# Optimization experiments

Measured on AMD Instinct MI355X. Metric: run time of the kernel, lower is better.

Reference implementation:

```python
import jax, jax.numpy as jnp
import numpy as np

NUM_HEADS = 16


def setup_inputs() -> dict:
    key = jax.random.key(0)
    k1, k2, k3 = jax.random.split(key, 3)
    B, S, D = 4, 2048, 1024
    x = jax.random.normal(k1, (B, S, D), dtype=jnp.float32)
    w_qkv = jax.random.normal(k2, (D, 3 * D), dtype=jnp.float32) * 0.02
    b_qkv = jnp.zeros((3 * D,), dtype=jnp.float32)
    w_proj = jax.random.normal(k3, (D, D), dtype=jnp.float32) * 0.02
    b_proj = jnp.zeros((D,), dtype=jnp.float32)
    return {"x": x, "w_qkv": w_qkv, "b_qkv": b_qkv, "w_proj": w_proj, "b_proj": b_proj}


def reference(x, w_qkv, b_qkv, w_proj, b_proj):
    B, S, D = x.shape
    H = NUM_HEADS
    hd = D // H
    # fused qkv projection: [B,S,3D] -> [B,S,3H,hd]
    qkv = (x @ w_qkv + b_qkv).reshape(B, S, 3 * H, hd)
    q, k, v = jnp.split(qkv, 3, axis=2)  # each [B,S,H,hd]
    scale = (1.0 / jnp.sqrt(hd)).astype(x.dtype)
    scores = jnp.einsum("bqhd,bkhd->bhqk", q, k) * scale  # [B,H,S,S]
    causal = jnp.tril(jnp.ones((S, S), dtype=bool))  # [S,S]
    masked = jnp.where(causal, scores, jnp.finfo(scores.dtype).min)
    # softmax in fp32 reduce dtype, cast back (dropout_rate=0 -> identity)
    attn = jax.nn.softmax(masked.astype(jnp.float32)).astype(masked.dtype)
    out = jnp.einsum("bhqk,bkhd->bqhd", attn, v).reshape(B, S, D)
    return out @ w_proj + b_proj
```

## Files before the change

### kernel.cpp

```cpp
#include <hip/hip_runtime.h>
#include <hip/hip_bf16.h>

typedef __attribute__((ext_vector_type(8))) short short8;
typedef __attribute__((ext_vector_type(4))) float f32x4;

#define B_   4
#define S_   2048
#define D_   1024
#define H_   16
#define HD_  64
#define M_   (B_ * S_)
#define N3_  (3 * D_)

#define GLDS16(g, l)                                                        \
  __builtin_amdgcn_global_load_lds(                                         \
      (const __attribute__((address_space(1))) void*)(g),                   \
      (__attribute__((address_space(3))) void*)(l), 16, 0, 0)

__device__ __forceinline__ unsigned pack_bf2(float a, float b) {
  union { __hip_bfloat16 h; unsigned short s; } ua, ub;
  ua.h = __float2bfloat16(a);
  ub.h = __float2bfloat16(b);
  return (unsigned)ua.s | ((unsigned)ub.s << 16);
}

__global__ __launch_bounds__(256) void cast_f32_bf16(
    const float* __restrict__ in, __hip_bfloat16* __restrict__ out, int n) {
  int i = (blockIdx.x * 256 + threadIdx.x) * 4;
  if (i + 3 < n) {
    float4 v = *(const float4*)(in + i);
    union { ushort4 u4; __hip_bfloat16 h[4]; } p;
    p.h[0] = __float2bfloat16(v.x);
    p.h[1] = __float2bfloat16(v.y);
    p.h[2] = __float2bfloat16(v.z);
    p.h[3] = __float2bfloat16(v.w);
    *(ushort4*)(out + i) = p.u4;
  }
}

__global__ __launch_bounds__(256) void transpose_cast(
    const float* __restrict__ in, __hip_bfloat16* __restrict__ out,
    int rows, int cols) {
  __shared__ float tile[32][33];
  int bx = blockIdx.x * 32;
  int by = blockIdx.y * 32;
  int tx = threadIdx.x, ty = threadIdx.y;
#pragma unroll
  for (int i = 0; i < 4; ++i)
    tile[ty + i * 8][tx] = in[(size_t)(by + ty + i * 8) * cols + bx + tx];
  __syncthreads();
#pragma unroll
  for (int i = 0; i < 4; ++i)
    out[(size_t)(bx + ty + i * 8) * rows + by + tx] =
        __float2bfloat16(tile[tx][ty + i * 8]);
}

__device__ inline void store_out(float* p, float v) { *p = v; }
__device__ inline void store_out(__hip_bfloat16* p, float v) {
  *p = __float2bfloat16(v);
}

template <typename OUT_T, bool WVT>
__global__ __launch_bounds__(256) void gemm_bt_bias(
    const __hip_bfloat16* __restrict__ A, const __hip_bfloat16* __restrict__ Bt,
    const float* __restrict__ bias, OUT_T* __restrict__ C,
    __hip_bfloat16* __restrict__ vt, int M, int N, int K) {
  __shared__ __align__(16) __hip_bfloat16 Alds[128 * 64];
  __shared__ __align__(16) __hip_bfloat16 Blds[128 * 64];
  const int t = threadIdx.x;
  const int wave = t >> 6, lane = t & 63;
  const int quad = lane >> 4, l15 = lane & 15;
  const int wm = (wave >> 1) * 64, wn = (wave & 1) * 64;
  const int m0 = blockIdx.y * 128, n0 = blockIdx.x * 128;

  const int rsub = lane >> 3;
  const int gc16 = (lane & 7) ^ (rsub & 7);
  const __hip_bfloat16* gA[4];
  const __hip_bfloat16* gB[4];
  __hip_bfloat16* lA[4];
  __hip_bfloat16* lB[4];
#pragma unroll
  for (int i = 0; i < 4; ++i) {
    int c = wave * 4 + i;
    int row = c * 8 + rsub;
    gA[i] = A + (size_t)(m0 + row) * K + gc16 * 8;
    gB[i] = Bt + (size_t)(n0 + row) * K + gc16 * 8;
    lA[i] = Alds + c * 512;
    lB[i] = Blds + c * 512;
  }

  f32x4 acc[4][4] = {};

  for (int k0 = 0; k0 < K; k0 += 64) {
#pragma unroll
    for (int i = 0; i < 4; ++i) {
      GLDS16(gA[i] + k0, lA[i]);
      GLDS16(gB[i] + k0, lB[i]);
    }
    __syncthreads();
#pragma unroll
    for (int kk = 0; kk < 2; ++kk) {
      const int fo = ((kk * 4 + quad) ^ (l15 & 7)) * 8;
      short8 a[4], bfr[4];
#pragma unroll
      for (int mt = 0; mt < 4; ++mt)
        a[mt] = *(const short8*)(Alds + (wm + mt * 16 + l15) * 64 + fo);
#pragma unroll
      for (int nt = 0; nt < 4; ++nt)
        bfr[nt] = *(const short8*)(Blds + (wn + nt * 16 + l15) * 64 + fo);
#pragma unroll
      for (int mt = 0; mt < 4; ++mt)
#pragma unroll
        for (int nt = 0; nt < 4; ++nt)
          acc[mt][nt] = __builtin_amdgcn_mfma_f32_16x16x32_bf16(
              a[mt], bfr[nt], acc[mt][nt], 0, 0, 0);
    }
    __syncthreads();
  }

  if (WVT && n0 >= 2048) {
#pragma unroll
    for (int mt = 0; mt < 4; ++mt)
#pragma unroll
      for (int nt = 0; nt < 4; ++nt) {
        int col = n0 + wn + nt * 16 + l15;
        float bv = bias[col];
        int hv = (col - 2048) >> 6, d = (col - 2048) & 63;
        int row0 = m0 + wm + mt * 16 + quad * 4;
        int bidx = row0 >> 11, s = row0 & 2047;
        uint2 w;
        w.x = pack_bf2(acc[mt][nt][0] + bv, acc[mt][nt][1] + bv);
        w.y = pack_bf2(acc[mt][nt][2] + bv, acc[mt][nt][3] + bv);
        *(uint2*)(vt + ((size_t)(bidx * 16 + hv) * 64 + d) * 2048 + s) = w;
      }
  } else {
#pragma unroll
    for (int mt = 0; mt < 4; ++mt)
#pragma unroll
      for (int nt = 0; nt < 4; ++nt) {
        int col = n0 + wn + nt * 16 + l15;
        float bv = bias[col];
#pragma unroll
        for (int r = 0; r < 4; ++r) {
          int row = m0 + wm + mt * 16 + quad * 4 + r;
          store_out(C + (size_t)row * N + col, acc[mt][nt][r] + bv);
        }
      }
  }
}

__global__ __launch_bounds__(128, 3) void attn_causal(
    const __hip_bfloat16* __restrict__ qkv,
    const __hip_bfloat16* __restrict__ vt,
    __hip_bfloat16* __restrict__ ctx) {
  __shared__ __align__(16) __hip_bfloat16 Klds[64 * 64];
  __shared__ __align__(16) __hip_bfloat16 Vlds[64 * 64];
  __shared__ __align__(16) __hip_bfloat16 Plds[2][2][16][64];

  const int t = threadIdx.x;
  const int wave = t >> 6, lane = t & 63;
  const int quad = lane >> 4, l15 = lane & 15;
  const int qb = 31 - (int)blockIdx.x;
  const int h = blockIdx.y, b = blockIdx.z;

  const size_t qbase = (size_t)b * S_ * N3_ + h * HD_;
  const size_t kbase = qbase + D_;
  const size_t vtbase = (size_t)(b * H_ + h) * HD_ * S_;
  const float C2 = 0.18033688f;

  short8 ones;
#pragma unroll
  for (int j = 0; j < 8; ++j) ones[j] = (short)0x3F80;

  short8 qf[2][2];
#pragma unroll
  for (int g = 0; g < 2; ++g) {
    const int qrow = qb * 64 + wave * 32 + g * 16 + l15;
    qf[g][0] = *(const short8*)(qkv + qbase + (size_t)qrow * N3_ + quad * 8);
    qf[g][1] =
        *(const short8*)(qkv + qbase + (size_t)qrow * N3_ + 32 + quad * 8);
  }

  const int rsub = lane >> 3;
  const int swz = ((lane & 7) ^ rsub) * 8;
  const __hip_bfloat16* gK[4];
  const __hip_bfloat16* gV[4];
  __hip_bfloat16* lK[4];
  __hip_bfloat16* lV[4];
#pragma unroll
  for (int i = 0; i < 4; ++i) {
    const int c = wave * 4 + i;
    gK[i] = qkv + kbase + (size_t)(c * 8 + rsub) * N3_ + swz;
    gV[i] = vt + vtbase + (size_t)(c * 8 + rsub) * S_ + swz;
    lK[i] = Klds + c * 512;
    lV[i] = Vlds + c * 512;
  }

  f32x4 o[2][4] = {};
  float m_r[2] = {-1e30f, -1e30f}, l_r[2] = {0.f, 0.f};

  const int fo0 = (quad ^ (l15 & 7)) * 8;
  const int fo1 = ((4 + quad) ^ (l15 & 7)) * 8;

#pragma unroll
  for (int i = 0; i < 4; ++i) {
    GLDS16(gK[i], lK[i]);
    GLDS16(gV[i], lV[i]);
  }
  __syncthreads();

  for (int kb = 0; kb <= qb; ++kb) {
    short8 kf[4][2], vf[4][2];
#pragma unroll
    for (int nt = 0; nt < 4; ++nt) {
      const __hip_bfloat16* kr = Klds + (nt * 16 + l15) * 64;
      const __hip_bfloat16* vr = Vlds + (nt * 16 + l15) * 64;
      kf[nt][0] = *(const short8*)(kr + fo0);
      kf[nt][1] = *(const short8*)(kr + fo1);
      vf[nt][0] = *(const short8*)(vr + fo0);
      vf[nt][1] = *(const short8*)(vr + fo1);
    }
    __syncthreads();
    if (kb < qb) {
#pragma unroll
      for (int i = 0; i < 4; ++i) {
        gK[i] += 64 * N3_;
        gV[i] += 64;
        GLDS16(gK[i], lK[i]);
        GLDS16(gV[i], lV[i]);
      }
    }

    const bool diag = (kb == qb);
    short8 pB[2][2];
#pragma unroll
    for (int g = 0; g < 2; ++g) {
      f32x4 st[4];
#pragma unroll
      for (int nt = 0; nt < 4; ++nt) {
        f32x4 z = {};
        z = __builtin_amdgcn_mfma_f32_16x16x32_bf16(kf[nt][0], qf[g][0], z,
                                                    0, 0, 0);
        z = __builtin_amdgcn_mfma_f32_16x16x32_bf16(kf[nt][1], qf[g][1], z,
                                                    0, 0, 0);
        st[nt] = z;
      }
      if (diag) {
        const int rloc = wave * 32 + g * 16 + l15;
#pragma unroll
        for (int nt = 0; nt < 4; ++nt)
#pragma unroll
          for (int r = 0; r < 4; ++r)
            if (nt * 16 + quad * 4 + r > rloc) st[nt][r] = -1e30f;
      }

      float tm = st[0][0];
#pragma unroll
      for (int nt = 0; nt < 4; ++nt)
#pragma unroll
        for (int r = 0; r < 4; ++r) tm = fmaxf(tm, st[nt][r]);
      tm = fmaxf(tm, __shfl_xor(tm, 16));
      tm = fmaxf(tm, __shfl_xor(tm, 32));
      const float pm = tm * C2;

      if (!__all(pm - m_r[g] <= 8.0f)) {
        const float mn = fmaxf(m_r[g], pm);
        const float al = __builtin_amdgcn_exp2f(m_r[g] - mn);
        m_r[g] = mn;
        l_r[g] *= al;
#pragma unroll
        for (int dt = 0; dt < 4; ++dt)
#pragma unroll
          for (int r = 0; r < 4; ++r) o[g][dt][r] *= al;
      }
      const float mneg = -m_r[g];

      __hip_bfloat16* prow = &Plds[wave][g][l15][0];
#pragma unroll
      for (int nt = 0; nt < 4; ++nt) {
        float p0 = __builtin_amdgcn_exp2f(__builtin_fmaf(st[nt][0], C2, mneg));
        float p1 = __builtin_amdgcn_exp2f(__builtin_fmaf(st[nt][1], C2, mneg));
        float p2 = __builtin_amdgcn_exp2f(__builtin_fmaf(st[nt][2], C2, mneg));
        float p3 = __builtin_amdgcn_exp2f(__builtin_fmaf(st[nt][3], C2, mneg));
        uint2 w;
        w.x = pack_bf2(p0, p1);
        w.y = pack_bf2(p2, p3);
        const int u = nt * 2 + (quad >> 1);
        *(uint2*)(prow + ((u ^ (l15 & 7)) * 8 + (quad & 1) * 4)) = w;
      }
      pB[g][0] = *(const short8*)(prow + fo0);
      pB[g][1] = *(const short8*)(prow + fo1);

      f32x4 ps = {};
      ps = __builtin_amdgcn_mfma_f32_16x16x32_bf16(ones, pB[g][0], ps, 0, 0, 0);
      ps = __builtin_amdgcn_mfma_f32_16x16x32_bf16(ones, pB[g][1], ps, 0, 0, 0);
      l_r[g] += ps[0];
    }

#pragma unroll
    for (int dt = 0; dt < 4; ++dt)
#pragma unroll
      for (int g = 0; g < 2; ++g) {
        o[g][dt] = __builtin_amdgcn_mfma_f32_16x16x32_bf16(vf[dt][0], pB[g][0],
                                                           o[g][dt], 0, 0, 0);
        o[g][dt] = __builtin_amdgcn_mfma_f32_16x16x32_bf16(vf[dt][1], pB[g][1],
                                                           o[g][dt], 0, 0, 0);
      }
    __syncthreads();
  }

#pragma unroll
  for (int g = 0; g < 2; ++g) {
    const float rl = __builtin_amdgcn_rcpf(l_r[g]);
    const int qrow = qb * 64 + wave * 32 + g * 16 + l15;
    __hip_bfloat16* crow = ctx + ((size_t)b * S_ + qrow) * D_ + h * HD_;
#pragma unroll
    for (int dt = 0; dt < 4; ++dt) {
      uint2 w;
      w.x = pack_bf2(o[g][dt][0] * rl, o[g][dt][1] * rl);
      w.y = pack_bf2(o[g][dt][2] * rl, o[g][dt][3] * rl);
      *(uint2*)(crow + dt * 16 + quad * 4) = w;
    }
  }
}

extern "C" void kernel_launch(void* const* d_in, const int* in_sizes, int n_in,
                              void* d_out, int out_size, void* d_ws,
                              size_t ws_size, hipStream_t stream) {
  const float* x      = (const float*)d_in[0];
  const float* w_qkv  = (const float*)d_in[1];
  const float* b_qkv  = (const float*)d_in[2];
  const float* w_proj = (const float*)d_in[3];
  const float* b_proj = (const float*)d_in[4];
  float* out = (float*)d_out;

  char* ws = (char*)d_ws;
  __hip_bfloat16* xb     = (__hip_bfloat16*)(ws + 0);
  __hip_bfloat16* wqkvT  = (__hip_bfloat16*)(ws + 16777216);
  __hip_bfloat16* wprojT = (__hip_bfloat16*)(ws + 23068672);
  __hip_bfloat16* qkvb   = (__hip_bfloat16*)(ws + 25165824);
  __hip_bfloat16* ctx    = (__hip_bfloat16*)(ws + 75497472);
  __hip_bfloat16* vt2    = (__hip_bfloat16*)(ws + 91750400);

  cast_f32_bf16<<<8192, 256, 0, stream>>>(x, xb, M_ * D_);
  transpose_cast<<<dim3(N3_ / 32, D_ / 32), dim3(32, 8), 0, stream>>>(
      w_qkv, wqkvT, D_, N3_);
  transpose_cast<<<dim3(D_ / 32, D_ / 32), dim3(32, 8), 0, stream>>>(
      w_proj, wprojT, D_, D_);

  gemm_bt_bias<__hip_bfloat16, true>
      <<<dim3(N3_ / 128, M_ / 128), 256, 0, stream>>>(
          xb, wqkvT, b_qkv, qkvb, vt2, M_, N3_, D_);

  attn_causal<<<dim3(32, H_, B_), 128, 0, stream>>>(qkvb, vt2, ctx);

  gemm_bt_bias<float, false><<<dim3(D_ / 128, M_ / 128), 256, 0, stream>>>(
      ctx, wprojT, b_proj, out, (__hip_bfloat16*)nullptr, M_, D_, D_);
}
```

Measured before the change: 309.8 us.

## Pair causal query blocks per workgroup and double-buffer K/V tiles in LDS

Each attention workgroup now handles two query blocks, xb and 31-xb, so every block does the same amount of causal work and the grid shrinks to 16 blocks along x. K/V tiles are double-buffered in LDS: the next tile's global-to-LDS load is issued before computing on the current one, which removes one barrier per iteration. The prefetch continues across the boundary between the two query blocks by reloading tile 0. LDS use doubles and launch bounds drop to 2 blocks per SM, which reduces occupancy and total block count in exchange for balanced work and overlapped loads.

```diff
diff --git a/kernel.cpp b/kernel.cpp
--- a/kernel.cpp
+++ b/kernel.cpp
@@ -149,19 +149,18 @@
   }
 }
 
-__global__ __launch_bounds__(128, 3) void attn_causal(
+__global__ __launch_bounds__(128, 2) void attn_causal(
     const __hip_bfloat16* __restrict__ qkv,
     const __hip_bfloat16* __restrict__ vt,
     __hip_bfloat16* __restrict__ ctx) {
-  __shared__ __align__(16) __hip_bfloat16 Klds[64 * 64];
-  __shared__ __align__(16) __hip_bfloat16 Vlds[64 * 64];
+  __shared__ __align__(16) __hip_bfloat16 Klds[2][64 * 64];
+  __shared__ __align__(16) __hip_bfloat16 Vlds[2][64 * 64];
   __shared__ __align__(16) __hip_bfloat16 Plds[2][2][16][64];
 
   const int t = threadIdx.x;
   const int wave = t >> 6, lane = t & 63;
   const int quad = lane >> 4, l15 = lane & 15;
-  const int qb = 31 - (int)blockIdx.x;
-  const int h = blockIdx.y, b = blockIdx.z;
+  const int xb = blockIdx.x, h = blockIdx.y, b = blockIdx.z;
 
   const size_t qbase = (size_t)b * S_ * N3_ + h * HD_;
   const size_t kbase = qbase + D_;
@@ -172,13 +171,18 @@
 #pragma unroll
   for (int j = 0; j < 8; ++j) ones[j] = (short)0x3F80;
 
-  short8 qf[2][2];
-#pragma unroll
-  for (int g = 0; g < 2; ++g) {
-    const int qrow = qb * 64 + wave * 32 + g * 16 + l15;
-    qf[g][0] = *(const short8*)(qkv + qbase + (size_t)qrow * N3_ + quad * 8);
-    qf[g][1] =
-        *(const short8*)(qkv + qbase + (size_t)qrow * N3_ + 32 + quad * 8);
+  short8 qf[2][2][2];
+#pragma unroll
+  for (int sel = 0; sel < 2; ++sel) {
+    const int qb = sel ? 31 - xb : xb;
+#pragma unroll
+    for (int g = 0; g < 2; ++g) {
+      const int qrow = qb * 64 + wave * 32 + g * 16 + l15;
+      qf[sel][g][0] =
+          *(const short8*)(qkv + qbase + (size_t)qrow * N3_ + quad * 8);
+      qf[sel][g][1] =
+          *(const short8*)(qkv + qbase + (size_t)qrow * N3_ + 32 + quad * 8);
+    }
   }
 
   const int rsub = lane >> 3;
@@ -192,12 +196,9 @@
     const int c = wave * 4 + i;
     gK[i] = qkv + kbase + (size_t)(c * 8 + rsub) * N3_ + swz;
     gV[i] = vt + vtbase + (size_t)(c * 8 + rsub) * S_ + swz;
-    lK[i] = Klds + c * 512;
-    lV[i] = Vlds + c * 512;
-  }
-
-  f32x4 o[2][4] = {};
-  float m_r[2] = {-1e30f, -1e30f}, l_r[2] = {0.f, 0.f};
+    lK[i] = &Klds[0][c * 512];
+    lV[i] = &Vlds[0][c * 512];
+  }
 
   const int fo0 = (quad ^ (l15 & 7)) * 8;
   const int fo1 = ((4 + quad) ^ (l15 & 7)) * 8;
@@ -208,118 +209,143 @@
     GLDS16(gV[i], lV[i]);
   }
   __syncthreads();
-
-  for (int kb = 0; kb <= qb; ++kb) {
-    short8 kf[4][2], vf[4][2];
-#pragma unroll
-    for (int nt = 0; nt < 4; ++nt) {
-      const __hip_bfloat16* kr = Klds + (nt * 16 + l15) * 64;
-      const __hip_bfloat16* vr = Vlds + (nt * 16 + l15) * 64;
-      kf[nt][0] = *(const short8*)(kr + fo0);
-      kf[nt][1] = *(const short8*)(kr + fo1);
-      vf[nt][0] = *(const short8*)(vr + fo0);
-      vf[nt][1] = *(const short8*)(vr + fo1);
-    }
-    __syncthreads();
-    if (kb < qb) {
-#pragma unroll
-      for (int i = 0; i < 4; ++i) {
-        gK[i] += 64 * N3_;
-        gV[i] += 64;
-        GLDS16(gK[i], lK[i]);
-        GLDS16(gV[i], lV[i]);
-      }
-    }
-
-    const bool diag = (kb == qb);
-    short8 pB[2][2];
+  int cur = 0;
+
+  for (int sel = 0; sel < 2; ++sel) {
+    const int qb = sel ? 31 - xb : xb;
+
+    f32x4 o[2][4] = {};
+    float m_r[2] = {-1e30f, -1e30f}, l_r[2] = {0.f, 0.f};
+
+    for (int kb = 0; kb <= qb; ++kb) {
+      if (sel == 0 || kb < qb) {
+        const size_t nk = (kb < qb) ? (size_t)(kb + 1) : 0;
+        const size_t ko = nk * (size_t)(64 * N3_);
+        const size_t vo = nk * 64;
+        const int nb = (cur ^ 1) * 4096;
+#pragma unroll
+        for (int i = 0; i < 4; ++i) {
+          GLDS16(gK[i] + ko, lK[i] + nb);
+          GLDS16(gV[i] + vo, lV[i] + nb);
+        }
+      }
+
+      const __hip_bfloat16* Kb = &Klds[cur][0];
+      const __hip_bfloat16* Vb = &Vlds[cur][0];
+
+      short8 kf[4][2];
+#pragma unroll
+      for (int nt = 0; nt < 4; ++nt) {
+        const __hip_bfloat16* kr = Kb + (nt * 16 + l15) * 64;
+        kf[nt][0] = *(const short8*)(kr + fo0);
+        kf[nt][1] = *(const short8*)(kr + fo1);
+      }
+
+      const bool diag = (kb == qb);
+      short8 pB[2][2];
+#pragma unroll
+      for (int g = 0; g < 2; ++g) {
+        f32x4 st[4];
+#pragma unroll
+        for (int nt = 0; nt < 4; ++nt) {
+          f32x4 z = {};
+          z = __builtin_amdgcn_mfma_f32_16x16x32_bf16(kf[nt][0], qf[sel][g][0],
+                                                      z, 0, 0, 0);
+          z = __builtin_amdgcn_mfma_f32_16x16x32_bf16(kf[nt][1], qf[sel][g][1],
+                                                      z, 0, 0, 0);
+          st[nt] = z;
+        }
+        if (diag) {
+          const int rloc = wave * 32 + g * 16 + l15;
+#pragma unroll
+          for (int nt = 0; nt < 4; ++nt)
+#pragma unroll
+            for (int r = 0; r < 4; ++r)
+              if (nt * 16 + quad * 4 + r > rloc) st[nt][r] = -1e30f;
+        }
+
+        float tm = st[0][0];
+#pragma unroll
+        for (int nt = 0; nt < 4; ++nt)
+#pragma unroll
+          for (int r = 0; r < 4; ++r) tm = fmaxf(tm, st[nt][r]);
+        tm = fmaxf(tm, __shfl_xor(tm, 16));
+        tm = fmaxf(tm, __shfl_xor(tm, 32));
+        const float pm = tm * C2;
+
+        if (!__all(pm - m_r[g] <= 8.0f)) {
+          const float mn = fmaxf(m_r[g], pm);
+          const float al = __builtin_amdgcn_exp2f(m_r[g] - mn);
+          m_r[g] = mn;
+          l_r[g] *= al;
+#pragma unroll
+          for (int dt = 0; dt < 4; ++dt)
+#pragma unroll
+            for (int r = 0; r < 4; ++r) o[g][dt][r] *= al;
+        }
+        const float mneg = -m_r[g];
+
+        __hip_bfloat16* prow = &Plds[wave][g][l15][0];
+#pragma unroll
+        for (int nt = 0; nt < 4; ++nt) {
+          float p0 =
+              __builtin_amdgcn_exp2f(__builtin_fmaf(st[nt][0], C2, mneg));
+          float p1 =
+              __builtin_amdgcn_exp2f(__builtin_fmaf(st[nt][1], C2, mneg));
+          float p2 =
+              __builtin_amdgcn_exp2f(__builtin_fmaf(st[nt][2], C2, mneg));
+          float p3 =
+              __builtin_amdgcn_exp2f(__builtin_fmaf(st[nt][3], C2, mneg));
+          uint2 w;
+          w.x = pack_bf2(p0, p1);
+          w.y = pack_bf2(p2, p3);
+          const int u = nt * 2 + (quad >> 1);
+          *(uint2*)(prow + ((u ^ (l15 & 7)) * 8 + (quad & 1) * 4)) = w;
+        }
+        pB[g][0] = *(const short8*)(prow + fo0);
+        pB[g][1] = *(const short8*)(prow + fo1);
+
+        f32x4 ps = {};
+        ps = __builtin_amdgcn_mfma_f32_16x16x32_bf16(ones, pB[g][0], ps,
+                                                     0, 0, 0);
+        ps = __builtin_amdgcn_mfma_f32_16x16x32_bf16(ones, pB[g][1], ps,
+                                                     0, 0, 0);
+        l_r[g] += ps[0];
+      }
+
+      short8 vf[4][2];
+#pragma unroll
+      for (int dt = 0; dt < 4; ++dt) {
+        const __hip_bfloat16* vr = Vb + (dt * 16 + l15) * 64;
+        vf[dt][0] = *(const short8*)(vr + fo0);
+        vf[dt][1] = *(const short8*)(vr + fo1);
+      }
+#pragma unroll
+      for (int dt = 0; dt < 4; ++dt)
+#pragma unroll
+        for (int g = 0; g < 2; ++g) {
+          o[g][dt] = __builtin_amdgcn_mfma_f32_16x16x32_bf16(
+              vf[dt][0], pB[g][0], o[g][dt], 0, 0, 0);
+          o[g][dt] = __builtin_amdgcn_mfma_f32_16x16x32_bf16(
+              vf[dt][1], pB[g][1], o[g][dt], 0, 0, 0);
+        }
+
+      __syncthreads();
+      cur ^= 1;
+    }
+
 #pragma unroll
     for (int g = 0; g < 2; ++g) {
-      f32x4 st[4];
-#pragma unroll
-      for (int nt = 0; nt < 4; ++nt) {
-        f32x4 z = {};
-        z = __builtin_amdgcn_mfma_f32_16x16x32_bf16(kf[nt][0], qf[g][0], z,
-                                                    0, 0, 0);
-        z = __builtin_amdgcn_mfma_f32_16x16x32_bf16(kf[nt][1], qf[g][1], z,
-                                                    0, 0, 0);
-        st[nt] = z;
-      }
-      if (diag) {
-        const int rloc = wave * 32 + g * 16 + l15;
-#pragma unroll
-        for (int nt = 0; nt < 4; ++nt)
-#pragma unroll
-          for (int r = 0; r < 4; ++r)
-            if (nt * 16 + quad * 4 + r > rloc) st[nt][r] = -1e30f;
-      }
-
-      float tm = st[0][0];
-#pragma unroll
-      for (int nt = 0; nt < 4; ++nt)
-#pragma unroll
-        for (int r = 0; r < 4; ++r) tm = fmaxf(tm, st[nt][r]);
-      tm = fmaxf(tm, __shfl_xor(tm, 16));
-      tm = fmaxf(tm, __shfl_xor(tm, 32));
-      const float pm = tm * C2;
-
-      if (!__all(pm - m_r[g] <= 8.0f)) {
-        const float mn = fmaxf(m_r[g], pm);
-        const float al = __builtin_amdgcn_exp2f(m_r[g] - mn);
-        m_r[g] = mn;
-        l_r[g] *= al;
-#pragma unroll
-        for (int dt = 0; dt < 4; ++dt)
-#pragma unroll
-          for (int r = 0; r < 4; ++r) o[g][dt][r] *= al;
-      }
-      const float mneg = -m_r[g];
-
-      __hip_bfloat16* prow = &Plds[wave][g][l15][0];
-#pragma unroll
-      for (int nt = 0; nt < 4; ++nt) {
-        float p0 = __builtin_amdgcn_exp2f(__builtin_fmaf(st[nt][0], C2, mneg));
-        float p1 = __builtin_amdgcn_exp2f(__builtin_fmaf(st[nt][1], C2, mneg));
-        float p2 = __builtin_amdgcn_exp2f(__builtin_fmaf(st[nt][2], C2, mneg));
-        float p3 = __builtin_amdgcn_exp2f(__builtin_fmaf(st[nt][3], C2, mneg));
+      const float rl = __builtin_amdgcn_rcpf(l_r[g]);
+      const int qrow = qb * 64 + wave * 32 + g * 16 + l15;
+      __hip_bfloat16* crow = ctx + ((size_t)b * S_ + qrow) * D_ + h * HD_;
+#pragma unroll
+      for (int dt = 0; dt < 4; ++dt) {
         uint2 w;
-        w.x = pack_bf2(p0, p1);
-        w.y = pack_bf2(p2, p3);
-        const int u = nt * 2 + (quad >> 1);
-        *(uint2*)(prow + ((u ^ (l15 & 7)) * 8 + (quad & 1) * 4)) = w;
-      }
-      pB[g][0] = *(const short8*)(prow + fo0);
-      pB[g][1] = *(const short8*)(prow + fo1);
-
-      f32x4 ps = {};
-      ps = __builtin_amdgcn_mfma_f32_16x16x32_bf16(ones, pB[g][0], ps, 0, 0, 0);
-      ps = __builtin_amdgcn_mfma_f32_16x16x32_bf16(ones, pB[g][1], ps, 0, 0, 0);
-      l_r[g] += ps[0];
-    }
-
-#pragma unroll
-    for (int dt = 0; dt < 4; ++dt)
-#pragma unroll
-      for (int g = 0; g < 2; ++g) {
-        o[g][dt] = __builtin_amdgcn_mfma_f32_16x16x32_bf16(vf[dt][0], pB[g][0],
-                                                           o[g][dt], 0, 0, 0);
-        o[g][dt] = __builtin_amdgcn_mfma_f32_16x16x32_bf16(vf[dt][1], pB[g][1],
-                                                           o[g][dt], 0, 0, 0);
-      }
-    __syncthreads();
-  }
-
-#pragma unroll
-  for (int g = 0; g < 2; ++g) {
-    const float rl = __builtin_amdgcn_rcpf(l_r[g]);
-    const int qrow = qb * 64 + wave * 32 + g * 16 + l15;
-    __hip_bfloat16* crow = ctx + ((size_t)b * S_ + qrow) * D_ + h * HD_;
-#pragma unroll
-    for (int dt = 0; dt < 4; ++dt) {
-      uint2 w;
-      w.x = pack_bf2(o[g][dt][0] * rl, o[g][dt][1] * rl);
-      w.y = pack_bf2(o[g][dt][2] * rl, o[g][dt][3] * rl);
-      *(uint2*)(crow + dt * 16 + quad * 4) = w;
+        w.x = pack_bf2(o[g][dt][0] * rl, o[g][dt][1] * rl);
+        w.y = pack_bf2(o[g][dt][2] * rl, o[g][dt][3] * rl);
+        *(uint2*)(crow + dt * 16 + quad * 4) = w;
+      }
     }
   }
 }
@@ -352,7 +378,7 @@
       <<<dim3(N3_ / 128, M_ / 128), 256, 0, stream>>>(
           xb, wqkvT, b_qkv, qkvb, vt2, M_, N3_, D_);
 
-  attn_causal<<<dim3(32, H_, B_), 128, 0, stream>>>(qkvb, vt2, ctx);
+  attn_causal<<<dim3(16, H_, B_), 128, 0, stream>>>(qkvb, vt2, ctx);
 
   gemm_bt_bias<float, false><<<dim3(D_ / 128, M_ / 128), 256, 0, stream>>>(
       ctx, wprojT, b_proj, out, (__hip_bfloat16*)nullptr, M_, D_, D_);
```

Result: faster. 295.4 us (-4.7%).
